# Performance work log

Hardware: AMD Instinct MI355X
Metric: run time of the kernel (lower is better)

The kernel has to match this reference:

```python
import jax, jax.numpy as jnp
import numpy as np

# YOLOv2 COCO anchors (w, h) in cell units
ANCHORS = np.array([[0.57273, 0.677385],
                    [1.87446, 2.06253],
                    [3.33843, 5.47434],
                    [7.88282, 3.52778],
                    [9.77052, 9.16828]], dtype=np.float32)

N, S, A, C = 16, 52, 5, 80
L_XY, L_WH, L_OBJ, L_NOOBJ, L_CLS = 5.0, 5.0, 1.0, 0.5, 1.0


def setup_inputs() -> dict:
    key = jax.random.key(0)
    k1, k2 = jax.random.split(key)
    pred = jax.random.normal(k1, (N, S, S, A, 5 + C), dtype=jnp.float32)
    target = jax.random.uniform(k2, (N, S, S, A, 5 + C), dtype=jnp.float32)
    return {"pred": pred, "target": target}


def _pairwise_iou(g, p):
    # g: [..., Agt, 4] gt boxes (cx, cy, w, h); p: [..., Apred, 4]
    g = g[..., :, None, :]   # [..., Agt, 1, 4]
    p = p[..., None, :, :]   # [..., 1, Apred, 4]
    g_x1, g_y1 = g[..., 0] - g[..., 2] / 2, g[..., 1] - g[..., 3] / 2
    g_x2, g_y2 = g[..., 0] + g[..., 2] / 2, g[..., 1] + g[..., 3] / 2
    p_x1, p_y1 = p[..., 0] - p[..., 2] / 2, p[..., 1] - p[..., 3] / 2
    p_x2, p_y2 = p[..., 0] + p[..., 2] / 2, p[..., 1] + p[..., 3] / 2
    iw = jnp.clip(jnp.minimum(g_x2, p_x2) - jnp.maximum(g_x1, p_x1), 0)
    ih = jnp.clip(jnp.minimum(g_y2, p_y2) - jnp.maximum(g_y1, p_y1), 0)
    inter = iw * ih
    union = (g_x2 - g_x1) * (g_y2 - g_y1) + (p_x2 - p_x1) * (p_y2 - p_y1) - inter + 1e-9
    return inter / union  # [..., Agt, Apred]


def reference(pred, target):
    anchors = jnp.asarray(ANCHORS, dtype=pred.dtype)
    aw, ah = anchors[:, 0], anchors[:, 1]  # broadcast over trailing anchor dim

    sx = jax.nn.sigmoid(pred[..., 0])
    sy = jax.nn.sigmoid(pred[..., 1])
    p_tw, p_th, p_to = pred[..., 2], pred[..., 3], pred[..., 4]
    pred_cls = pred[..., 5:]

    # decoded boxes, [N,S,S,A,4]
    p_box = jnp.stack([sx, sy, jnp.exp(p_tw) * aw, jnp.exp(p_th) * ah], axis=-1)
    g_box = jnp.stack([target[..., 0], target[..., 1],
                       jnp.exp(target[..., 2]) * aw,
                       jnp.exp(target[..., 3]) * ah], axis=-1)

    ious = _pairwise_iou(g_box, p_box)  # [N,S,S,Agt,Apred]

    # sequential greedy anchor assignment per cell (A is small and fixed)
    taken = jnp.zeros(pred.shape[:4], dtype=bool)          # [N,S,S,A]
    aligned = jnp.zeros_like(target)                       # [N,S,S,A,5+C]
    ar = jnp.arange(A)
    for a in range(A):
        valid = target[..., a, 4] > 0.5                    # [N,S,S]
        row = jnp.where(taken, -1.0, ious[..., a, :])      # [N,S,S,A]
        best = jnp.argmax(row, axis=-1)                    # [N,S,S]
        sel = (ar == best[..., None]) & valid[..., None]   # [N,S,S,A]
        taken = taken | sel
        aligned = jnp.where(sel[..., None], target[..., a, :][..., None, :], aligned)

    obj = aligned[..., 4] > 0.5                            # [N,S,S,A]
    objf = obj.astype(pred.dtype)

    loss_xy = L_XY * jnp.sum(objf * ((sx - aligned[..., 0]) ** 2 + (sy - aligned[..., 1]) ** 2))
    loss_wh = L_WH * jnp.sum(objf * ((p_tw - aligned[..., 2]) ** 2 + (p_th - aligned[..., 3]) ** 2))
    loss_obj = L_OBJ * jnp.sum(objf * jax.nn.softplus(-p_to))
    loss_noobj = L_NOOBJ * jnp.sum((1.0 - objf) * jax.nn.softplus(p_to))

    logp = jax.nn.log_softmax(pred_cls, axis=-1)
    labels = jnp.argmax(aligned[..., 5:], axis=-1)
    nll = -jnp.take_along_axis(logp, labels[..., None], axis=-1)[..., 0]
    loss_cls = L_CLS * jnp.sum(objf * nll)

    total = (loss_xy + loss_wh + loss_obj + loss_noobj + loss_cls) / pred.shape[0]
    return total
```

## Files before the change

### kernel.cpp

```cpp
#include <hip/hip_runtime.h>
#include <math.h>
#include <stdint.h>


#define NIMG   16
#define NA     5
#define NC     80
#define STRIDE 85
#define CELLF  (NA * STRIDE)
#define NCELLS 43264
#define NANCH  (NCELLS * NA)

#define K1_CELLS   64
#define K1_THREADS 320
#define K1_BLOCKS  (NCELLS / K1_CELLS)
#define K3_BLOCKS  (NANCH / 16)
#define NPART      (K1_BLOCKS + K3_BLOCKS)

__device__ __constant__ float AW[5] = {0.57273f, 1.87446f, 3.33843f, 7.88282f, 9.77052f};
__device__ __constant__ float AH[5] = {0.677385f, 2.06253f, 5.47434f, 3.52778f, 9.16828f};

__device__ inline float softplusf(float x) {
    return fmaxf(x, 0.0f) + log1pf(expf(-fabsf(x)));
}
__device__ inline float sigmoidf(float x) { return 1.0f / (1.0f + expf(-x)); }

__global__ __launch_bounds__(K1_THREADS) void yolo_k1(
    const float* __restrict__ pred, const float* __restrict__ target,
    uint32_t* __restrict__ assign_ws, float* __restrict__ part_ws) {
    __shared__ float s_px1[K1_THREADS], s_px2[K1_THREADS], s_py1[K1_THREADS], s_py2[K1_THREADS], s_pA[K1_THREADS];
    __shared__ float s_gx1[K1_THREADS], s_gx2[K1_THREADS], s_gy1[K1_THREADS], s_gy2[K1_THREADS], s_gA[K1_THREADS];
    __shared__ float s_gobj[K1_THREADS];
    __shared__ float s_sx[K1_THREADS], s_sy[K1_THREADS], s_ptw[K1_THREADS], s_pth[K1_THREADS];
    __shared__ float s_spn[K1_THREADS], s_spp[K1_THREADS];
    __shared__ float s_tx[K1_THREADS], s_ty[K1_THREADS], s_tw[K1_THREADS], s_th[K1_THREADS];

    const int t = threadIdx.x;
    const int ga = blockIdx.x * K1_THREADS + t;
    const int a = t % NA;
    const float* pa = pred   + (size_t)ga * STRIDE;
    const float* ta = target + (size_t)ga * STRIDE;
    const float p0 = pa[0], p1 = pa[1], p2 = pa[2], p3 = pa[3], p4 = pa[4];
    const float t0 = ta[0], t1 = ta[1], t2 = ta[2], t3 = ta[3], t4 = ta[4];
    const float aw = AW[a], ah = AH[a];

    const float sx = sigmoidf(p0);
    const float sy = sigmoidf(p1);
    const float pw = expf(p2) * aw, ph = expf(p3) * ah;
    const float gw = expf(t2) * aw, gh = expf(t3) * ah;

    s_px1[t] = sx - pw * 0.5f;  s_px2[t] = sx + pw * 0.5f;
    s_py1[t] = sy - ph * 0.5f;  s_py2[t] = sy + ph * 0.5f;
    s_pA[t]  = pw * ph;
    s_gx1[t] = t0 - gw * 0.5f;  s_gx2[t] = t0 + gw * 0.5f;
    s_gy1[t] = t1 - gh * 0.5f;  s_gy2[t] = t1 + gh * 0.5f;
    s_gA[t]  = gw * gh;
    s_gobj[t] = t4;
    s_sx[t] = sx;  s_sy[t] = sy;  s_ptw[t] = p2;  s_pth[t] = p3;
    s_spn[t] = softplusf(-p4);    s_spp[t] = softplusf(p4);
    s_tx[t] = t0;  s_ty[t] = t1;  s_tw[t] = t2;  s_th[t] = t3;
    __syncthreads();

    float cellLoss = 0.0f;
    if (t < 64) {
        const int la = t * NA;
        float iou[NA][NA];
#pragma unroll
        for (int g = 0; g < NA; ++g) {
            const float gx1 = s_gx1[la+g], gx2 = s_gx2[la+g];
            const float gy1 = s_gy1[la+g], gy2 = s_gy2[la+g];
            const float gA  = s_gA[la+g];
#pragma unroll
            for (int p = 0; p < NA; ++p) {
                float iw = fmaxf(fminf(gx2, s_px2[la+p]) - fmaxf(gx1, s_px1[la+p]), 0.0f);
                float ih = fmaxf(fminf(gy2, s_py2[la+p]) - fmaxf(gy1, s_py1[la+p]), 0.0f);
                float inter = iw * ih;
                iou[g][p] = inter / (gA + s_pA[la+p] - inter + 1e-9f);
            }
        }
        int assign[NA] = {-1, -1, -1, -1, -1};
        bool taken[NA] = {false, false, false, false, false};
#pragma unroll
        for (int g = 0; g < NA; ++g) {
            if (s_gobj[la+g] > 0.5f) {
                float best = -2.0f; int bi = 0;
#pragma unroll
                for (int p = 0; p < NA; ++p) {
                    float v = taken[p] ? -1.0f : iou[g][p];
                    if (v > best) { best = v; bi = p; }
                }
                taken[bi] = true;
                assign[bi] = g;
            }
        }
        uint32_t word = 0;
        float l_xy = 0.f, l_wh = 0.f, l_obj = 0.f, l_noobj = 0.f;
#pragma unroll
        for (int p = 0; p < NA; ++p) {
            const int g = assign[p];
            word |= (uint32_t)(g + 1) << (4 * p);
            if (g >= 0) {
                float dx = s_sx[la+p] - s_tx[la+g];
                float dy = s_sy[la+p] - s_ty[la+g];
                l_xy += dx * dx + dy * dy;
                float dw = s_ptw[la+p] - s_tw[la+g];
                float dh = s_pth[la+p] - s_th[la+g];
                l_wh += dw * dw + dh * dh;
                l_obj += s_spn[la+p];
            } else {
                l_noobj += s_spp[la+p];
            }
        }
        assign_ws[blockIdx.x * K1_CELLS + t] = word;
        cellLoss = 5.0f * l_xy + 5.0f * l_wh + 1.0f * l_obj + 0.5f * l_noobj;
#pragma unroll
        for (int o = 32; o; o >>= 1) cellLoss += __shfl_xor(cellLoss, o);
        if (t == 0) part_ws[blockIdx.x] = cellLoss;
    }
}

__global__ __launch_bounds__(256) void yolo_k3(
    const float* __restrict__ pred, const float* __restrict__ target,
    const uint32_t* __restrict__ assign_ws, float* __restrict__ part_ws) {
    __shared__ float wsum[4];
    const int tid  = threadIdx.x;
    const int gi   = blockIdx.x * 16 + (tid >> 4);
    const int lane = tid & 15;
    const int c = gi / NA;
    const int p = gi - c * NA;
    const int g = (int)((assign_ws[c] >> (4 * p)) & 0xFu) - 1;

    float contrib = 0.0f;
    if (g >= 0) {
        const float* pc = pred   + (size_t)c * CELLF + p * STRIDE + 5;
        const float* tc = target + (size_t)c * CELLF + g * STRIDE + 5;
        float pv[5], tv[5];
#pragma unroll
        for (int k = 0; k < 5; ++k) {
            pv[k] = pc[lane + 16 * k];
            tv[k] = tc[lane + 16 * k];
        }
        float m = fmaxf(fmaxf(fmaxf(pv[0], pv[1]), fmaxf(pv[2], pv[3])), pv[4]);
#pragma unroll
        for (int o = 1; o < 16; o <<= 1) m = fmaxf(m, __shfl_xor(m, o));
        float s = 0.f;
#pragma unroll
        for (int k = 0; k < 5; ++k) s += expf(pv[k] - m);
#pragma unroll
        for (int o = 1; o < 16; o <<= 1) s += __shfl_xor(s, o);
        float lse = m + logf(s);

        float bt = tv[0]; int bi = lane; float bp = pv[0];
#pragma unroll
        for (int k = 1; k < 5; ++k) {
            if (tv[k] > bt) { bt = tv[k]; bi = lane + 16 * k; bp = pv[k]; }
        }
#pragma unroll
        for (int o = 1; o < 16; o <<= 1) {
            float ot = __shfl_xor(bt, o);
            int   oi = __shfl_xor(bi, o);
            float op = __shfl_xor(bp, o);
            if (ot > bt || (ot == bt && oi < bi)) { bt = ot; bi = oi; bp = op; }
        }
        contrib = (lane == 0) ? (lse - bp) : 0.0f;
    }
    contrib += __shfl_xor(contrib, 16);
    contrib += __shfl_xor(contrib, 32);
    if ((tid & 63) == 0) wsum[tid >> 6] = contrib;
    __syncthreads();
    if (tid == 0)
        part_ws[K1_BLOCKS + blockIdx.x] = wsum[0] + wsum[1] + wsum[2] + wsum[3];
}

__global__ __launch_bounds__(256) void yolo_k4(
    const float* __restrict__ part_ws, float* __restrict__ out) {
    __shared__ float ws4[4];
    float s = 0.0f;
    for (int i = threadIdx.x; i < NPART; i += 256) s += part_ws[i];
#pragma unroll
    for (int o = 32; o; o >>= 1) s += __shfl_xor(s, o);
    if ((threadIdx.x & 63) == 0) ws4[threadIdx.x >> 6] = s;
    __syncthreads();
    if (threadIdx.x == 0)
        out[0] = (ws4[0] + ws4[1] + ws4[2] + ws4[3]) * (1.0f / (float)NIMG);
}

extern "C" void kernel_launch(void* const* d_in, const int* in_sizes, int n_in,
                              void* d_out, int out_size, void* d_ws, size_t ws_size,
                              hipStream_t stream) {
    const float* pred   = (const float*)d_in[0];
    const float* target = (const float*)d_in[1];
    float* out = (float*)d_out;
    uint32_t* assign_ws = (uint32_t*)d_ws;
    float* part_ws = (float*)d_ws + NCELLS;

    yolo_k1<<<K1_BLOCKS, K1_THREADS, 0, stream>>>(pred, target, assign_ws, part_ws);
    yolo_k3<<<K3_BLOCKS, 256, 0, stream>>>(pred, target, assign_ws, part_ws);
    yolo_k4<<<1, 256, 0, stream>>>(part_ws, out);
}
```

Baseline: 183.9 us.

## Fuse anchor assignment and class-loss kernels into one block-local kernel

Merges the box/assignment kernel and the class cross-entropy kernel into one kernel that handles 32 cells per 256-thread block. The assignment words stay in shared memory instead of going through a global workspace, and one launch is dropped. Each 16-lane group now walks 10 anchor slots in sequence. This lowers parallelism per block, and only 160 of 256 threads take part in the load phase.

```diff
diff --git a/kernel.cpp b/kernel.cpp
--- a/kernel.cpp
+++ b/kernel.cpp
@@ -5,17 +5,13 @@
 
 #define NIMG   16
 #define NA     5
-#define NC     80
 #define STRIDE 85
 #define CELLF  (NA * STRIDE)
 #define NCELLS 43264
-#define NANCH  (NCELLS * NA)
-
-#define K1_CELLS   64
-#define K1_THREADS 320
-#define K1_BLOCKS  (NCELLS / K1_CELLS)
-#define K3_BLOCKS  (NANCH / 16)
-#define NPART      (K1_BLOCKS + K3_BLOCKS)
+#define CPB    32
+#define BT     256
+#define NANCHB (CPB * NA)
+#define NB     (NCELLS / CPB)
 
 __device__ __constant__ float AW[5] = {0.57273f, 1.87446f, 3.33843f, 7.88282f, 9.77052f};
 __device__ __constant__ float AH[5] = {0.677385f, 2.06253f, 5.47434f, 3.52778f, 9.16828f};
@@ -25,44 +21,49 @@
 }
 __device__ inline float sigmoidf(float x) { return 1.0f / (1.0f + expf(-x)); }
 
-__global__ __launch_bounds__(K1_THREADS) void yolo_k1(
+__global__ __launch_bounds__(BT) void yolo_fused(
     const float* __restrict__ pred, const float* __restrict__ target,
-    uint32_t* __restrict__ assign_ws, float* __restrict__ part_ws) {
-    __shared__ float s_px1[K1_THREADS], s_px2[K1_THREADS], s_py1[K1_THREADS], s_py2[K1_THREADS], s_pA[K1_THREADS];
-    __shared__ float s_gx1[K1_THREADS], s_gx2[K1_THREADS], s_gy1[K1_THREADS], s_gy2[K1_THREADS], s_gA[K1_THREADS];
-    __shared__ float s_gobj[K1_THREADS];
-    __shared__ float s_sx[K1_THREADS], s_sy[K1_THREADS], s_ptw[K1_THREADS], s_pth[K1_THREADS];
-    __shared__ float s_spn[K1_THREADS], s_spp[K1_THREADS];
-    __shared__ float s_tx[K1_THREADS], s_ty[K1_THREADS], s_tw[K1_THREADS], s_th[K1_THREADS];
+    float* __restrict__ part_ws) {
+    __shared__ float s_px1[NANCHB], s_px2[NANCHB], s_py1[NANCHB], s_py2[NANCHB], s_pA[NANCHB];
+    __shared__ float s_gx1[NANCHB], s_gx2[NANCHB], s_gy1[NANCHB], s_gy2[NANCHB], s_gA[NANCHB];
+    __shared__ float s_gobj[NANCHB];
+    __shared__ float s_sx[NANCHB], s_sy[NANCHB], s_ptw[NANCHB], s_pth[NANCHB];
+    __shared__ float s_spn[NANCHB], s_spp[NANCHB];
+    __shared__ float s_tx[NANCHB], s_ty[NANCHB], s_tw[NANCHB], s_th[NANCHB];
+    __shared__ uint32_t s_assign[CPB];
+    __shared__ float s_wpart[BT / 64];
 
     const int t = threadIdx.x;
-    const int ga = blockIdx.x * K1_THREADS + t;
-    const int a = t % NA;
-    const float* pa = pred   + (size_t)ga * STRIDE;
-    const float* ta = target + (size_t)ga * STRIDE;
-    const float p0 = pa[0], p1 = pa[1], p2 = pa[2], p3 = pa[3], p4 = pa[4];
-    const float t0 = ta[0], t1 = ta[1], t2 = ta[2], t3 = ta[3], t4 = ta[4];
-    const float aw = AW[a], ah = AH[a];
 
-    const float sx = sigmoidf(p0);
-    const float sy = sigmoidf(p1);
-    const float pw = expf(p2) * aw, ph = expf(p3) * ah;
-    const float gw = expf(t2) * aw, gh = expf(t3) * ah;
+    if (t < NANCHB) {
+        const int ga = blockIdx.x * NANCHB + t;
+        const int a = t % NA;
+        const float* pa = pred   + (size_t)ga * STRIDE;
+        const float* ta = target + (size_t)ga * STRIDE;
+        const float p0 = pa[0], p1 = pa[1], p2 = pa[2], p3 = pa[3], p4 = pa[4];
+        const float t0 = ta[0], t1 = ta[1], t2 = ta[2], t3 = ta[3], t4 = ta[4];
+        const float aw = AW[a], ah = AH[a];
 
-    s_px1[t] = sx - pw * 0.5f;  s_px2[t] = sx + pw * 0.5f;
-    s_py1[t] = sy - ph * 0.5f;  s_py2[t] = sy + ph * 0.5f;
-    s_pA[t]  = pw * ph;
-    s_gx1[t] = t0 - gw * 0.5f;  s_gx2[t] = t0 + gw * 0.5f;
-    s_gy1[t] = t1 - gh * 0.5f;  s_gy2[t] = t1 + gh * 0.5f;
-    s_gA[t]  = gw * gh;
-    s_gobj[t] = t4;
-    s_sx[t] = sx;  s_sy[t] = sy;  s_ptw[t] = p2;  s_pth[t] = p3;
-    s_spn[t] = softplusf(-p4);    s_spp[t] = softplusf(p4);
-    s_tx[t] = t0;  s_ty[t] = t1;  s_tw[t] = t2;  s_th[t] = t3;
+        const float sx = sigmoidf(p0);
+        const float sy = sigmoidf(p1);
+        const float pw = expf(p2) * aw, ph = expf(p3) * ah;
+        const float gw = expf(t2) * aw, gh = expf(t3) * ah;
+
+        s_px1[t] = sx - pw * 0.5f;  s_px2[t] = sx + pw * 0.5f;
+        s_py1[t] = sy - ph * 0.5f;  s_py2[t] = sy + ph * 0.5f;
+        s_pA[t]  = pw * ph;
+        s_gx1[t] = t0 - gw * 0.5f;  s_gx2[t] = t0 + gw * 0.5f;
+        s_gy1[t] = t1 - gh * 0.5f;  s_gy2[t] = t1 + gh * 0.5f;
+        s_gA[t]  = gw * gh;
+        s_gobj[t] = t4;
+        s_sx[t] = sx;  s_sy[t] = sy;  s_ptw[t] = p2;  s_pth[t] = p3;
+        s_spn[t] = softplusf(-p4);    s_spp[t] = softplusf(p4);
+        s_tx[t] = t0;  s_ty[t] = t1;  s_tw[t] = t2;  s_th[t] = t3;
+    }
     __syncthreads();
 
-    float cellLoss = 0.0f;
-    if (t < 64) {
+    float loss = 0.0f;
+    if (t < CPB) {
         const int la = t * NA;
         float iou[NA][NA];
 #pragma unroll
@@ -111,72 +112,68 @@
                 l_noobj += s_spp[la+p];
             }
         }
-        assign_ws[blockIdx.x * K1_CELLS + t] = word;
-        cellLoss = 5.0f * l_xy + 5.0f * l_wh + 1.0f * l_obj + 0.5f * l_noobj;
+        s_assign[t] = word;
+        loss = 5.0f * l_xy + 5.0f * l_wh + 1.0f * l_obj + 0.5f * l_noobj;
+    }
+    __syncthreads();
+
+    const int grp = t >> 4;
+    const int ln  = t & 15;
 #pragma unroll
-        for (int o = 32; o; o >>= 1) cellLoss += __shfl_xor(cellLoss, o);
-        if (t == 0) part_ws[blockIdx.x] = cellLoss;
+    for (int si = 0; si < 10; ++si) {
+        const int slot = grp * 10 + si;
+        const int cell = slot / NA;
+        const int p    = slot - cell * NA;
+        const int g    = (int)((s_assign[cell] >> (4 * p)) & 0xFu) - 1;
+        if (g >= 0) {
+            const size_t cbase = ((size_t)blockIdx.x * CPB + cell) * CELLF;
+            const float* pc = pred   + cbase + p * STRIDE + 5;
+            const float* tc = target + cbase + g * STRIDE + 5;
+            float pv[5], tv[5];
+#pragma unroll
+            for (int k = 0; k < 5; ++k) {
+                pv[k] = pc[ln + 16 * k];
+                tv[k] = tc[ln + 16 * k];
+            }
+            float m = fmaxf(fmaxf(fmaxf(pv[0], pv[1]), fmaxf(pv[2], pv[3])), pv[4]);
+#pragma unroll
+            for (int o = 1; o < 16; o <<= 1) m = fmaxf(m, __shfl_xor(m, o));
+            float s = 0.f;
+#pragma unroll
+            for (int k = 0; k < 5; ++k) s += expf(pv[k] - m);
+#pragma unroll
+            for (int o = 1; o < 16; o <<= 1) s += __shfl_xor(s, o);
+            float lse = m + logf(s);
+
+            float bt = tv[0]; int bi = ln; float bp = pv[0];
+#pragma unroll
+            for (int k = 1; k < 5; ++k) {
+                if (tv[k] > bt) { bt = tv[k]; bi = ln + 16 * k; bp = pv[k]; }
+            }
+#pragma unroll
+            for (int o = 1; o < 16; o <<= 1) {
+                float ot = __shfl_xor(bt, o);
+                int   oi = __shfl_xor(bi, o);
+                float op = __shfl_xor(bp, o);
+                if (ot > bt || (ot == bt && oi < bi)) { bt = ot; bi = oi; bp = op; }
+            }
+            if (ln == 0) loss += lse - bp;
+        }
     }
+
+#pragma unroll
+    for (int o = 32; o; o >>= 1) loss += __shfl_xor(loss, o);
+    if ((t & 63) == 0) s_wpart[t >> 6] = loss;
+    __syncthreads();
+    if (t == 0)
+        part_ws[blockIdx.x] = s_wpart[0] + s_wpart[1] + s_wpart[2] + s_wpart[3];
 }
 
-__global__ __launch_bounds__(256) void yolo_k3(
-    const float* __restrict__ pred, const float* __restrict__ target,
-    const uint32_t* __restrict__ assign_ws, float* __restrict__ part_ws) {
-    __shared__ float wsum[4];
-    const int tid  = threadIdx.x;
-    const int gi   = blockIdx.x * 16 + (tid >> 4);
-    const int lane = tid & 15;
-    const int c = gi / NA;
-    const int p = gi - c * NA;
-    const int g = (int)((assign_ws[c] >> (4 * p)) & 0xFu) - 1;
-
-    float contrib = 0.0f;
-    if (g >= 0) {
-        const float* pc = pred   + (size_t)c * CELLF + p * STRIDE + 5;
-        const float* tc = target + (size_t)c * CELLF + g * STRIDE + 5;
-        float pv[5], tv[5];
-#pragma unroll
-        for (int k = 0; k < 5; ++k) {
-            pv[k] = pc[lane + 16 * k];
-            tv[k] = tc[lane + 16 * k];
-        }
-        float m = fmaxf(fmaxf(fmaxf(pv[0], pv[1]), fmaxf(pv[2], pv[3])), pv[4]);
-#pragma unroll
-        for (int o = 1; o < 16; o <<= 1) m = fmaxf(m, __shfl_xor(m, o));
-        float s = 0.f;
-#pragma unroll
-        for (int k = 0; k < 5; ++k) s += expf(pv[k] - m);
-#pragma unroll
-        for (int o = 1; o < 16; o <<= 1) s += __shfl_xor(s, o);
-        float lse = m + logf(s);
-
-        float bt = tv[0]; int bi = lane; float bp = pv[0];
-#pragma unroll
-        for (int k = 1; k < 5; ++k) {
-            if (tv[k] > bt) { bt = tv[k]; bi = lane + 16 * k; bp = pv[k]; }
-        }
-#pragma unroll
-        for (int o = 1; o < 16; o <<= 1) {
-            float ot = __shfl_xor(bt, o);
-            int   oi = __shfl_xor(bi, o);
-            float op = __shfl_xor(bp, o);
-            if (ot > bt || (ot == bt && oi < bi)) { bt = ot; bi = oi; bp = op; }
-        }
-        contrib = (lane == 0) ? (lse - bp) : 0.0f;
-    }
-    contrib += __shfl_xor(contrib, 16);
-    contrib += __shfl_xor(contrib, 32);
-    if ((tid & 63) == 0) wsum[tid >> 6] = contrib;
-    __syncthreads();
-    if (tid == 0)
-        part_ws[K1_BLOCKS + blockIdx.x] = wsum[0] + wsum[1] + wsum[2] + wsum[3];
-}
-
-__global__ __launch_bounds__(256) void yolo_k4(
+__global__ __launch_bounds__(256) void yolo_reduce(
     const float* __restrict__ part_ws, float* __restrict__ out) {
     __shared__ float ws4[4];
     float s = 0.0f;
-    for (int i = threadIdx.x; i < NPART; i += 256) s += part_ws[i];
+    for (int i = threadIdx.x; i < NB; i += 256) s += part_ws[i];
 #pragma unroll
     for (int o = 32; o; o >>= 1) s += __shfl_xor(s, o);
     if ((threadIdx.x & 63) == 0) ws4[threadIdx.x >> 6] = s;
@@ -191,10 +188,8 @@
     const float* pred   = (const float*)d_in[0];
     const float* target = (const float*)d_in[1];
     float* out = (float*)d_out;
-    uint32_t* assign_ws = (uint32_t*)d_ws;
-    float* part_ws = (float*)d_ws + NCELLS;
+    float* part_ws = (float*)d_ws;
 
-    yolo_k1<<<K1_BLOCKS, K1_THREADS, 0, stream>>>(pred, target, assign_ws, part_ws);
-    yolo_k3<<<K3_BLOCKS, 256, 0, stream>>>(pred, target, assign_ws, part_ws);
-    yolo_k4<<<1, 256, 0, stream>>>(part_ws, out);
+    yolo_fused<<<NB, BT, 0, stream>>>(pred, target, part_ws);
+    yolo_reduce<<<1, 256, 0, stream>>>(part_ws, out);
 }
```

Result: faster. 170.1 us (-7.5%).
